# Kernel optimization log

Hardware: AMD Instinct MI355X
Metric: run time of the kernel (lower is better)

## Reference

```python
import jax, jax.numpy as jnp
import numpy as np

B, S, HID = 1, 2048, 4096
NH, NKV = 32, 8
HD = HID // NH            # 128
GROUPS = NH // NKV        # 4
ROPE_THETA = 10000.0


def _rope_cos_sin(seq_len, head_dim, dtype=jnp.float32):
    inv_freq = 1.0 / (ROPE_THETA ** (jnp.arange(0, head_dim, 2, dtype=jnp.float32) / head_dim))
    t = jnp.arange(seq_len, dtype=jnp.float32)
    freqs = jnp.outer(t, inv_freq)                      # [S, HD/2]
    emb = jnp.concatenate([freqs, freqs], axis=-1)      # [S, HD]
    return jnp.cos(emb).astype(dtype), jnp.sin(emb).astype(dtype)


def _rotate_half(x):
    x1, x2 = jnp.split(x, 2, axis=-1)
    return jnp.concatenate([-x2, x1], axis=-1)


def _apply_rope(x, cos, sin):
    # x: [B, H, S, HD]; cos/sin: [S, HD] (position_ids = arange(S), no past)
    return x * cos[None, None] + _rotate_half(x) * sin[None, None]


def setup_inputs() -> dict:
    key = jax.random.key(0)
    k1, k2, k3, k4, k5 = jax.random.split(key, 5)
    return {
        "hidden_states": jax.random.normal(k1, (B, S, HID), jnp.float32),
        "Wq": jax.random.normal(k2, (NH * HD, HID), jnp.float32) * 0.02,
        "Wk": jax.random.normal(k3, (NKV * HD, HID), jnp.float32) * 0.02,
        "Wv": jax.random.normal(k4, (NKV * HD, HID), jnp.float32) * 0.02,
        "Wo": jax.random.normal(k5, (HID, NH * HD), jnp.float32) * 0.02,
    }


def reference(hidden_states, Wq, Wk, Wv, Wo):
    bsz, q_len, _ = hidden_states.shape
    # projections (nn.Linear: x @ W.T)
    q = (hidden_states @ Wq.T).reshape(bsz, q_len, NH, HD).transpose(0, 2, 1, 3)   # [B,NH,S,HD]
    k = (hidden_states @ Wk.T).reshape(bsz, q_len, NKV, HD).transpose(0, 2, 1, 3)  # [B,NKV,S,HD]
    v = (hidden_states @ Wv.T).reshape(bsz, q_len, NKV, HD).transpose(0, 2, 1, 3)

    cos, sin = _rope_cos_sin(q_len, HD, hidden_states.dtype)
    q = _apply_rope(q, cos, sin)
    k = _apply_rope(k, cos, sin)

    # GQA: repeat kv heads (repeat_kv / num_key_value_groups)
    k = jnp.repeat(k, GROUPS, axis=1)   # [B,NH,S,HD]
    v = jnp.repeat(v, GROUPS, axis=1)

    scale = 1.0 / jnp.sqrt(jnp.asarray(HD, hidden_states.dtype))
    logits = jnp.einsum('bhqd,bhkd->bhqk', q, k) * scale   # [B,NH,S,S]

    # prefill causal mask (phys_past_len = 0)
    causal = jnp.tril(jnp.ones((q_len, q_len), dtype=bool))
    logits = jnp.where(causal[None, None], logits, jnp.finfo(logits.dtype).min)

    attn = jax.nn.softmax(logits, axis=-1)
    out = jnp.einsum('bhqk,bhkd->bhqd', attn, v)            # [B,NH,S,HD]
    out = out.transpose(0, 2, 1, 3).reshape(bsz, q_len, NH * HD)
    return out @ Wo.T
```

## Files before the change

kernel.cpp:

```cpp
#include <hip/hip_runtime.h>

typedef __bf16 bf16;
typedef __bf16 bf16x2 __attribute__((ext_vector_type(2)));
typedef __bf16 bf16x4 __attribute__((ext_vector_type(4)));
typedef __bf16 bf16x8 __attribute__((ext_vector_type(8)));
typedef float f32x4 __attribute__((ext_vector_type(4)));

#define S_LEN 2048
#define HID_DIM 4096
#define NH 32
#define NKV 8
#define HD 128
#define QKV_N 6144
#define K_COL 4096
#define V_COL 5120
#define PADV 76

__global__ void cvt_all_kernel(const float* __restrict__ hs, const float* __restrict__ wq,
                               const float* __restrict__ wk, const float* __restrict__ wv,
                               const float* __restrict__ wo, bf16* __restrict__ hsb,
                               bf16* __restrict__ wqkvb, bf16* __restrict__ wob) {
  long i = (long)blockIdx.x * blockDim.x + threadIdx.x;
  const float* src; bf16* dst; long off;
  if (i < 2097152)      { src = hs; dst = hsb;                          off = i; }
  else if (i < 6291456) { src = wq; dst = wqkvb;                        off = i - 2097152; }
  else if (i < 7340032) { src = wk; dst = wqkvb + (long)4096 * 4096;    off = i - 6291456; }
  else if (i < 8388608) { src = wv; dst = wqkvb + (long)5120 * 4096;    off = i - 7340032; }
  else                  { src = wo; dst = wob;                          off = i - 8388608; }
  float4 v = reinterpret_cast<const float4*>(src)[off];
  bf16x4 o;
  o[0] = (bf16)v.x; o[1] = (bf16)v.y; o[2] = (bf16)v.z; o[3] = (bf16)v.w;
  reinterpret_cast<bf16x4*>(dst)[off] = o;
}

__global__ void rope_table_kernel(float* __restrict__ cost, float* __restrict__ sint) {
  int i = blockIdx.x * blockDim.x + threadIdx.x;
  int s = i >> 6, d = i & 63;
  float inv = expf(-0.14391156831212787f * (float)d);
  float ang = (float)s * inv;
  cost[i] = cosf(ang);
  sint[i] = sinf(ang);
}

__global__ void rope_apply_kernel(bf16* __restrict__ qkv, const float* __restrict__ cost,
                                  const float* __restrict__ sint) {
  int idx = blockIdx.x * blockDim.x + threadIdx.x;
  int s = idx / 320;
  int c = idx - s * 320;
  int g = c >> 3, dc = (c & 7) * 8;
  long base = (long)s * QKV_N + g * 128 + dc;
  bf16x8 x1 = *reinterpret_cast<const bf16x8*>(qkv + base);
  bf16x8 x2 = *reinterpret_cast<const bf16x8*>(qkv + base + 64);
  const float* cp = cost + (s << 6) + dc;
  const float* sp = sint + (s << 6) + dc;
  float4 ca = *reinterpret_cast<const float4*>(cp);
  float4 cb = *reinterpret_cast<const float4*>(cp + 4);
  float4 sa = *reinterpret_cast<const float4*>(sp);
  float4 sb = *reinterpret_cast<const float4*>(sp + 4);
  float co[8] = {ca.x, ca.y, ca.z, ca.w, cb.x, cb.y, cb.z, cb.w};
  float sn[8] = {sa.x, sa.y, sa.z, sa.w, sb.x, sb.y, sb.z, sb.w};
  bf16x8 y1, y2;
#pragma unroll
  for (int e = 0; e < 8; ++e) {
    float a = (float)x1[e], b = (float)x2[e];
    y1[e] = (bf16)(a * co[e] - b * sn[e]);
    y2[e] = (bf16)(b * co[e] + a * sn[e]);
  }
  *reinterpret_cast<bf16x8*>(qkv + base)      = y1;
  *reinterpret_cast<bf16x8*>(qkv + base + 64) = y2;
}

#define STG8(buf, mat, kt, unit) {                                                       \
    const bf16* sp_ = (mat) ? Bp : Ap;                                                   \
    int row0_ = ((mat) ? n0 : m0) + (unit) * 64;                                         \
    int lb_ = (buf) * LBUF + (mat) * 16384 + (unit) * 4096;                              \
    int r_ = t >> 3, jl_ = t & 7, jg_ = jl_ ^ (r_ & 7);                                  \
    const bf16* src_ = sp_ + (long)(row0_ + r_) * K + (kt) * 64 + jg_ * 8;               \
    __builtin_amdgcn_global_load_lds((const __attribute__((address_space(1))) void*)src_,\
        (__attribute__((address_space(3))) void*)(L + lb_ + t * 8), 16, 0, 0); }

#define DSA8(buf, mh, ks) {                                                              \
    _Pragma("unroll") for (int mf_ = 0; mf_ < 4; ++mf_) {                                \
      int R_ = wr * 128 + (mh) * 64 + mf_ * 16 + lm;                                     \
      aF[mf_] = *reinterpret_cast<const bf16x8*>(                                        \
          L + (buf) * LBUF + R_ * 64 + ((((ks) * 4 + lg) ^ (R_ & 7)) << 3));             \
    } }

#define DSB8(buf) {                                                                      \
    _Pragma("unroll") for (int ks_ = 0; ks_ < 2; ++ks_)                                  \
      _Pragma("unroll") for (int nf_ = 0; nf_ < NB; ++nf_) {                             \
        int R_ = wc * (NB * 16) + nf_ * 16 + lm;                                         \
        bF[ks_][nf_] = *reinterpret_cast<const bf16x8*>(                                 \
            L + (buf) * LBUF + 16384 + R_ * 64 + (((ks_ * 4 + lg) ^ (R_ & 7)) << 3));    \
      } }

#define MM8(mh, ks) {                                                                    \
    __builtin_amdgcn_s_setprio(1);                                                       \
    _Pragma("unroll") for (int mf_ = 0; mf_ < 4; ++mf_)                                  \
      _Pragma("unroll") for (int nf_ = 0; nf_ < NB; ++nf_)                               \
        acc[(mh) * 4 + mf_][nf_] = __builtin_amdgcn_mfma_f32_16x16x32_bf16(              \
            aF[mf_], bF[ks][nf_], acc[(mh) * 4 + mf_][nf_], 0, 0, 0);                    \
    __builtin_amdgcn_s_setprio(0); }

#define BAR() __builtin_amdgcn_s_barrier()
#define WVM(n) asm volatile("s_waitcnt vmcnt(%0)" :: "i"(n) : "memory")

template<int NB, typename OutT>
__global__ __launch_bounds__(512, 1) void gemm8p_kernel(
    const bf16* __restrict__ Ap, const bf16* __restrict__ Bp, OutT* __restrict__ C,
    int M, int N, int K) {
  constexpr int LBUF = 16384 + NB * 4096;
  __shared__ __align__(16) bf16 L[2 * LBUF];

  int nwg = gridDim.x * gridDim.y;
  int bid = blockIdx.y * gridDim.x + blockIdx.x;
  int cpx = nwg >> 3;
  int swz = (bid & 7) * cpx + (bid >> 3);
  int bxs = swz % gridDim.x, bys = swz / gridDim.x;
  const int n0 = bxs * (NB * 64), m0 = bys * 256;

  const int t = threadIdx.x;
  const int lane = t & 63, w = t >> 6;
  const int wr = w >> 2, wc = w & 3;
  const int lg = lane >> 4, lm = lane & 15;
  const int NT = K >> 6;

  f32x4 acc[8][NB] = {};
  bf16x8 aF[4], bF[2][NB];

  STG8(0, 0, 0, 0); STG8(0, 0, 0, 1); STG8(0, 0, 0, 2); STG8(0, 0, 0, 3);
  STG8(0, 1, 0, 0); if (NB > 1) STG8(0, 1, 0, 1); if (NB > 2) STG8(0, 1, 0, 2);
  STG8(1, 1, 1, 0); if (NB > 1) STG8(1, 1, 1, 1); if (NB > 2) STG8(1, 1, 1, 2);
  WVM(NB);
  BAR();

  for (int I = 0; I < (NT >> 1); ++I) {
    const int tt = 2 * I;
    const bool pf = (I < (NT >> 1) - 1);
    DSA8(0, 0, 0); DSB8(0);
    STG8(1, 0, tt + 1, 0); STG8(1, 0, tt + 1, 1);
    BAR(); MM8(0, 0); BAR();
    DSA8(0, 1, 0);
    STG8(1, 0, tt + 1, 2); STG8(1, 0, tt + 1, 3);
    BAR(); MM8(1, 0); BAR();
    DSA8(0, 0, 1);
    if (pf) { STG8(0, 1, tt + 2, 0); if (NB > 1) STG8(0, 1, tt + 2, 1); }
    BAR(); MM8(0, 1); BAR();
    DSA8(0, 1, 1);
    if (pf) { if (NB > 2) STG8(0, 1, tt + 2, 2); }
    BAR(); MM8(1, 1);
    if (pf) WVM(NB); else WVM(0);
    BAR();
    DSA8(1, 0, 0); DSB8(1);
    if (pf) { STG8(0, 0, tt + 2, 0); STG8(0, 0, tt + 2, 1); }
    BAR(); MM8(0, 0); BAR();
    DSA8(1, 1, 0);
    if (pf) { STG8(0, 0, tt + 2, 2); STG8(0, 0, tt + 2, 3); }
    BAR(); MM8(1, 0); BAR();
    DSA8(1, 0, 1);
    if (pf) { STG8(1, 1, tt + 3, 0); if (NB > 1) STG8(1, 1, tt + 3, 1); }
    BAR(); MM8(0, 1); BAR();
    DSA8(1, 1, 1);
    if (pf) { if (NB > 2) STG8(1, 1, tt + 3, 2); }
    BAR(); MM8(1, 1);
    if (pf) WVM(NB); else WVM(0);
    BAR();
  }

#pragma unroll
  for (int am = 0; am < 8; ++am) {
    int row = m0 + wr * 128 + am * 16 + lg * 4;
#pragma unroll
    for (int nf = 0; nf < NB; ++nf) {
      int col = n0 + wc * (NB * 16) + nf * 16 + lm;
#pragma unroll
      for (int rr = 0; rr < 4; ++rr) {
        if constexpr (sizeof(OutT) == 4) C[(long)(row + rr) * N + col] = acc[am][nf][rr];
        else                             C[(long)(row + rr) * N + col] = (bf16)acc[am][nf][rr];
      }
    }
  }
}

__global__ __launch_bounds__(512, 4) void attn_kernel(const bf16* __restrict__ qkv,
                                                      bf16* __restrict__ out) {
  __shared__ __align__(16) bf16 Ks[2][64 * 128];
  __shared__ __align__(16) bf16 Vt[128 * PADV];

  const int bx = blockIdx.x;
  const int qt = 15 - (bx >> 5);
  const int h = bx & 31;
  const int kvh = h >> 2;
  const int q0 = qt * 128;
  const int t = threadIdx.x, lane = t & 63, w = t >> 6;
  const int lg = lane >> 4, lm = lane & 15;
  const int dchunk = t >> 5, kv2 = t & 31;
  const int kva = kv2 * 2;
  const int k5 = kva & 31;
  const int slot = ((kva >> 5) << 5) | (((k5 >> 2) & 3) << 3) | ((k5 >> 4) << 2) | (k5 & 3);
  const bf16* kbase = qkv + K_COL + kvh * HD;
  const bf16* vbase = qkv + V_COL + kvh * HD;

  const long qrow = q0 + w * 16 + lm;
  bf16x8 qf[4];
#pragma unroll
  for (int ks = 0; ks < 4; ++ks)
    qf[ks] = *reinterpret_cast<const bf16x8*>(qkv + qrow * QKV_N + h * HD + ks * 32 + lg * 8);

  f32x4 o[8];
#pragma unroll
  for (int i = 0; i < 8; ++i) o[i] = f32x4{0.f, 0.f, 0.f, 0.f};
  float mrow = -1e30f, lrow = 0.f;

  bf16x8 a0, a1;
  {
#pragma unroll
    for (int i = 0; i < 2; ++i) {
      int c = i * 512 + t;
      int r = c >> 4, jl = c & 15;
      int jg = jl ^ (r & 15);
      const bf16* src = kbase + (long)r * QKV_N + jg * 8;
      __builtin_amdgcn_global_load_lds((const __attribute__((address_space(1))) void*)src,
                                       (__attribute__((address_space(3))) void*)(Ks[0] + c * 8), 16, 0, 0);
    }
    const bf16* vs = vbase + (long)kva * QKV_N + dchunk * 8;
    a0 = *reinterpret_cast<const bf16x8*>(vs);
    a1 = *reinterpret_cast<const bf16x8*>(vs + QKV_N);
  }

  const int nst = 2 * qt + 2;
  for (int st = 0; st < nst; ++st) {
    const int cur = st & 1;
#pragma unroll
    for (int e = 0; e < 8; ++e) {
      bf16x2 pk; pk[0] = a0[e]; pk[1] = a1[e];
      *reinterpret_cast<bf16x2*>(Vt + (dchunk * 8 + e) * PADV + slot) = pk;
    }
    __syncthreads();

    if (st + 1 < nst) {
      const long kv0n = (long)(st + 1) * 64;
#pragma unroll
      for (int i = 0; i < 2; ++i) {
        int c = i * 512 + t;
        int r = c >> 4, jl = c & 15;
        int jg = jl ^ (r & 15);
        const bf16* src = kbase + (kv0n + r) * QKV_N + jg * 8;
        __builtin_amdgcn_global_load_lds((const __attribute__((address_space(1))) void*)src,
                                         (__attribute__((address_space(3))) void*)(Ks[cur ^ 1] + c * 8), 16, 0, 0);
      }
      const bf16* vs = vbase + (kv0n + kva) * QKV_N + dchunk * 8;
      a0 = *reinterpret_cast<const bf16x8*>(vs);
      a1 = *reinterpret_cast<const bf16x8*>(vs + QKV_N);
    }

    const int kv0 = st * 64;
    const int qg = q0 + w * 16 + lm;
    if (kv0 <= q0 + w * 16 + 15) {
      f32x4 s[4];
#pragma unroll
      for (int cb = 0; cb < 4; ++cb) s[cb] = f32x4{0.f, 0.f, 0.f, 0.f};
      __builtin_amdgcn_s_setprio(1);
#pragma unroll
      for (int ks = 0; ks < 4; ++ks) {
#pragma unroll
        for (int cb = 0; cb < 4; ++cb) {
          bf16x8 kf = *reinterpret_cast<const bf16x8*>(
              Ks[cur] + (cb * 16 + lm) * 128 + (((ks * 4 + lg) ^ lm) << 3));
          s[cb] = __builtin_amdgcn_mfma_f32_16x16x32_bf16(kf, qf[ks], s[cb], 0, 0, 0);
        }
      }
      __builtin_amdgcn_s_setprio(0);

      const float SC = 0.12751742f;
      float sl[4][4];
#pragma unroll
      for (int cb = 0; cb < 4; ++cb)
#pragma unroll
        for (int r = 0; r < 4; ++r) {
          float v = s[cb][r] * SC;
          if (st >= nst - 2 && (kv0 + cb * 16 + lg * 4 + r) > qg) v = -1e30f;
          sl[cb][r] = v;
        }
      float tm = sl[0][0];
#pragma unroll
      for (int cb = 0; cb < 4; ++cb)
#pragma unroll
        for (int r = 0; r < 4; ++r) tm = fmaxf(tm, sl[cb][r]);
      tm = fmaxf(tm, __shfl_xor(tm, 16));
      tm = fmaxf(tm, __shfl_xor(tm, 32));

      if (__any(tm > mrow + 8.f)) {
        float mnew = fmaxf(mrow, tm);
        float alpha = exp2f(mrow - mnew);
        mrow = mnew;
        lrow *= alpha;
        float ar[4];
#pragma unroll
        for (int r = 0; r < 4; ++r)
          ar[r] = __shfl(alpha, (lane & 48) | (lg * 4 + r));
#pragma unroll
        for (int i = 0; i < 8; ++i)
#pragma unroll
          for (int r = 0; r < 4; ++r) o[i][r] *= ar[r];
      }
      float p[4][4];
      float psum = 0.f;
#pragma unroll
      for (int cb = 0; cb < 4; ++cb)
#pragma unroll
        for (int r = 0; r < 4; ++r) {
          p[cb][r] = exp2f(sl[cb][r] - mrow);
          psum += p[cb][r];
        }
      psum += __shfl_xor(psum, 16);
      psum += __shfl_xor(psum, 32);
      lrow += psum;

      bf16x8 pa0, pa1;
#pragma unroll
      for (int r = 0; r < 4; ++r) {
        pa0[r]     = (bf16)p[0][r];
        pa0[4 + r] = (bf16)p[1][r];
        pa1[r]     = (bf16)p[2][r];
        pa1[4 + r] = (bf16)p[3][r];
      }

      __builtin_amdgcn_s_setprio(1);
#pragma unroll
      for (int db = 0; db < 8; ++db) {
        bf16x8 vf0 = *reinterpret_cast<const bf16x8*>(Vt + (db * 16 + lm) * PADV + lg * 8);
        bf16x8 vf1 = *reinterpret_cast<const bf16x8*>(Vt + (db * 16 + lm) * PADV + 32 + lg * 8);
        o[db] = __builtin_amdgcn_mfma_f32_16x16x32_bf16(pa0, vf0, o[db], 0, 0, 0);
        o[db] = __builtin_amdgcn_mfma_f32_16x16x32_bf16(pa1, vf1, o[db], 0, 0, 0);
      }
      __builtin_amdgcn_s_setprio(0);
    }

    if (st + 1 < nst) __syncthreads();
  }

  float invr[4];
#pragma unroll
  for (int r = 0; r < 4; ++r)
    invr[r] = 1.0f / __shfl(lrow, (lane & 48) | (lg * 4 + r));
#pragma unroll
  for (int r = 0; r < 4; ++r) {
    long row = q0 + w * 16 + lg * 4 + r;
#pragma unroll
    for (int db = 0; db < 8; ++db)
      out[row * HID_DIM + h * HD + db * 16 + lm] = (bf16)(o[db][r] * invr[r]);
  }
}

extern "C" void kernel_launch(void* const* d_in, const int* in_sizes, int n_in,
                              void* d_out, int out_size, void* d_ws, size_t ws_size,
                              hipStream_t stream) {
  const float* hs = (const float*)d_in[0];
  const float* Wq = (const float*)d_in[1];
  const float* Wk = (const float*)d_in[2];
  const float* Wv = (const float*)d_in[3];
  const float* Wo = (const float*)d_in[4];
  float* out = (float*)d_out;
  char* ws = (char*)d_ws;

  bf16*  hsb   = (bf16*)(ws);
  bf16*  wqkvb = (bf16*)(ws + 16777216);
  bf16*  wob   = (bf16*)(ws + 67108864);
  bf16*  qkv   = (bf16*)(ws + 100663296);
  bf16*  attn  = (bf16*)(ws + 125829120);
  float* cost  = (float*)(ws + 142606336);
  float* sint  = (float*)(ws + 143130624);

  cvt_all_kernel<<<49152, 256, 0, stream>>>(hs, Wq, Wk, Wv, Wo, hsb, wqkvb, wob);
  rope_table_kernel<<<512, 256, 0, stream>>>(cost, sint);
  gemm8p_kernel<3, bf16><<<dim3(32, 8), 512, 0, stream>>>(hsb, wqkvb, qkv, 2048, 6144, 4096);
  rope_apply_kernel<<<2560, 256, 0, stream>>>(qkv, cost, sint);
  attn_kernel<<<512, 512, 0, stream>>>(qkv, attn);
  gemm8p_kernel<2, float><<<dim3(32, 8), 512, 0, stream>>>(attn, wob, out, 2048, 4096, 4096);
}
```

Before: 310.7 us.

## Cut GEMM pipeline to four phases per K-pair and fuse rope table into convert

The GEMM main loop now loads both k-subslices of A fragments at once and issues MFMAs over both, so each 64-wide K tile needs two barrier-separated phases instead of four. Global-to-LDS prefetches are regrouped to match the new phases. This halves the number of workgroup barriers and LDS-read phases, but raises register pressure because the A fragments double. The rope cos/sin table computation is also folded into the conversion kernel, which removes one kernel launch.

```diff
diff --git a/kernel.cpp b/kernel.cpp
--- a/kernel.cpp
+++ b/kernel.cpp
@@ -19,8 +19,18 @@
 __global__ void cvt_all_kernel(const float* __restrict__ hs, const float* __restrict__ wq,
                                const float* __restrict__ wk, const float* __restrict__ wv,
                                const float* __restrict__ wo, bf16* __restrict__ hsb,
-                               bf16* __restrict__ wqkvb, bf16* __restrict__ wob) {
+                               bf16* __restrict__ wqkvb, bf16* __restrict__ wob,
+                               float* __restrict__ cost, float* __restrict__ sint) {
   long i = (long)blockIdx.x * blockDim.x + threadIdx.x;
+  if (i >= 12582912) {
+    int j = (int)(i - 12582912);
+    int s = j >> 6, d = j & 63;
+    float inv = expf(-0.14391156831212787f * (float)d);
+    float ang = (float)s * inv;
+    cost[j] = cosf(ang);
+    sint[j] = sinf(ang);
+    return;
+  }
   const float* src; bf16* dst; long off;
   if (i < 2097152)      { src = hs; dst = hsb;                          off = i; }
   else if (i < 6291456) { src = wq; dst = wqkvb;                        off = i - 2097152; }
@@ -31,15 +41,6 @@
   bf16x4 o;
   o[0] = (bf16)v.x; o[1] = (bf16)v.y; o[2] = (bf16)v.z; o[3] = (bf16)v.w;
   reinterpret_cast<bf16x4*>(dst)[off] = o;
-}
-
-__global__ void rope_table_kernel(float* __restrict__ cost, float* __restrict__ sint) {
-  int i = blockIdx.x * blockDim.x + threadIdx.x;
-  int s = i >> 6, d = i & 63;
-  float inv = expf(-0.14391156831212787f * (float)d);
-  float ang = (float)s * inv;
-  cost[i] = cosf(ang);
-  sint[i] = sinf(ang);
 }
 
 __global__ void rope_apply_kernel(bf16* __restrict__ qkv, const float* __restrict__ cost,
@@ -79,14 +80,15 @@
     __builtin_amdgcn_global_load_lds((const __attribute__((address_space(1))) void*)src_,\
         (__attribute__((address_space(3))) void*)(L + lb_ + t * 8), 16, 0, 0); }
 
-#define DSA8(buf, mh, ks) {                                                              \
-    _Pragma("unroll") for (int mf_ = 0; mf_ < 4; ++mf_) {                                \
-      int R_ = wr * 128 + (mh) * 64 + mf_ * 16 + lm;                                     \
-      aF[mf_] = *reinterpret_cast<const bf16x8*>(                                        \
-          L + (buf) * LBUF + R_ * 64 + ((((ks) * 4 + lg) ^ (R_ & 7)) << 3));             \
-    } }
-
-#define DSB8(buf) {                                                                      \
+#define DSA2(buf, mh) {                                                                  \
+    _Pragma("unroll") for (int ks_ = 0; ks_ < 2; ++ks_)                                  \
+      _Pragma("unroll") for (int mf_ = 0; mf_ < 4; ++mf_) {                              \
+        int R_ = wr * 128 + (mh) * 64 + mf_ * 16 + lm;                                   \
+        aF[ks_][mf_] = *reinterpret_cast<const bf16x8*>(                                 \
+            L + (buf) * LBUF + R_ * 64 + (((ks_ * 4 + lg) ^ (R_ & 7)) << 3));            \
+      } }
+
+#define DSBALL(buf) {                                                                    \
     _Pragma("unroll") for (int ks_ = 0; ks_ < 2; ++ks_)                                  \
       _Pragma("unroll") for (int nf_ = 0; nf_ < NB; ++nf_) {                             \
         int R_ = wc * (NB * 16) + nf_ * 16 + lm;                                         \
@@ -94,19 +96,20 @@
             L + (buf) * LBUF + 16384 + R_ * 64 + (((ks_ * 4 + lg) ^ (R_ & 7)) << 3));    \
       } }
 
-#define MM8(mh, ks) {                                                                    \
+#define MM2(mh) {                                                                        \
     __builtin_amdgcn_s_setprio(1);                                                       \
     _Pragma("unroll") for (int mf_ = 0; mf_ < 4; ++mf_)                                  \
       _Pragma("unroll") for (int nf_ = 0; nf_ < NB; ++nf_)                               \
-        acc[(mh) * 4 + mf_][nf_] = __builtin_amdgcn_mfma_f32_16x16x32_bf16(              \
-            aF[mf_], bF[ks][nf_], acc[(mh) * 4 + mf_][nf_], 0, 0, 0);                    \
+        _Pragma("unroll") for (int ks_ = 0; ks_ < 2; ++ks_)                              \
+          acc[(mh) * 4 + mf_][nf_] = __builtin_amdgcn_mfma_f32_16x16x32_bf16(            \
+              aF[ks_][mf_], bF[ks_][nf_], acc[(mh) * 4 + mf_][nf_], 0, 0, 0);            \
     __builtin_amdgcn_s_setprio(0); }
 
 #define BAR() __builtin_amdgcn_s_barrier()
 #define WVM(n) asm volatile("s_waitcnt vmcnt(%0)" :: "i"(n) : "memory")
 
 template<int NB, typename OutT>
-__global__ __launch_bounds__(512, 1) void gemm8p_kernel(
+__global__ __launch_bounds__(512, 1) void gemm4p_kernel(
     const bf16* __restrict__ Ap, const bf16* __restrict__ Bp, OutT* __restrict__ C,
     int M, int N, int K) {
   constexpr int LBUF = 16384 + NB * 4096;
@@ -126,7 +129,7 @@
   const int NT = K >> 6;
 
   f32x4 acc[8][NB] = {};
-  bf16x8 aF[4], bF[2][NB];
+  bf16x8 aF[2][4], bF[2][NB];
 
   STG8(0, 0, 0, 0); STG8(0, 0, 0, 1); STG8(0, 0, 0, 2); STG8(0, 0, 0, 3);
   STG8(0, 1, 0, 0); if (NB > 1) STG8(0, 1, 0, 1); if (NB > 2) STG8(0, 1, 0, 2);
@@ -137,32 +140,24 @@
   for (int I = 0; I < (NT >> 1); ++I) {
     const int tt = 2 * I;
     const bool pf = (I < (NT >> 1) - 1);
-    DSA8(0, 0, 0); DSB8(0);
+    DSA2(0, 0); DSBALL(0);
     STG8(1, 0, tt + 1, 0); STG8(1, 0, tt + 1, 1);
-    BAR(); MM8(0, 0); BAR();
-    DSA8(0, 1, 0);
     STG8(1, 0, tt + 1, 2); STG8(1, 0, tt + 1, 3);
-    BAR(); MM8(1, 0); BAR();
-    DSA8(0, 0, 1);
-    if (pf) { STG8(0, 1, tt + 2, 0); if (NB > 1) STG8(0, 1, tt + 2, 1); }
-    BAR(); MM8(0, 1); BAR();
-    DSA8(0, 1, 1);
-    if (pf) { if (NB > 2) STG8(0, 1, tt + 2, 2); }
-    BAR(); MM8(1, 1);
+    BAR(); MM2(0); BAR();
+    DSA2(0, 1);
+    if (pf) { STG8(0, 1, tt + 2, 0); if (NB > 1) STG8(0, 1, tt + 2, 1);
+              if (NB > 2) STG8(0, 1, tt + 2, 2); }
+    BAR(); MM2(1);
     if (pf) WVM(NB); else WVM(0);
     BAR();
-    DSA8(1, 0, 0); DSB8(1);
-    if (pf) { STG8(0, 0, tt + 2, 0); STG8(0, 0, tt + 2, 1); }
-    BAR(); MM8(0, 0); BAR();
-    DSA8(1, 1, 0);
-    if (pf) { STG8(0, 0, tt + 2, 2); STG8(0, 0, tt + 2, 3); }
-    BAR(); MM8(1, 0); BAR();
-    DSA8(1, 0, 1);
-    if (pf) { STG8(1, 1, tt + 3, 0); if (NB > 1) STG8(1, 1, tt + 3, 1); }
-    BAR(); MM8(0, 1); BAR();
-    DSA8(1, 1, 1);
-    if (pf) { if (NB > 2) STG8(1, 1, tt + 3, 2); }
-    BAR(); MM8(1, 1);
+    DSA2(1, 0); DSBALL(1);
+    if (pf) { STG8(0, 0, tt + 2, 0); STG8(0, 0, tt + 2, 1);
+              STG8(0, 0, tt + 2, 2); STG8(0, 0, tt + 2, 3); }
+    BAR(); MM2(0); BAR();
+    DSA2(1, 1);
+    if (pf) { STG8(1, 1, tt + 3, 0); if (NB > 1) STG8(1, 1, tt + 3, 1);
+              if (NB > 2) STG8(1, 1, tt + 3, 2); }
+    BAR(); MM2(1);
     if (pf) WVM(NB); else WVM(0);
     BAR();
   }
@@ -372,10 +367,9 @@
   float* cost  = (float*)(ws + 142606336);
   float* sint  = (float*)(ws + 143130624);
 
-  cvt_all_kernel<<<49152, 256, 0, stream>>>(hs, Wq, Wk, Wv, Wo, hsb, wqkvb, wob);
-  rope_table_kernel<<<512, 256, 0, stream>>>(cost, sint);
-  gemm8p_kernel<3, bf16><<<dim3(32, 8), 512, 0, stream>>>(hsb, wqkvb, qkv, 2048, 6144, 4096);
+  cvt_all_kernel<<<49664, 256, 0, stream>>>(hs, Wq, Wk, Wv, Wo, hsb, wqkvb, wob, cost, sint);
+  gemm4p_kernel<3, bf16><<<dim3(32, 8), 512, 0, stream>>>(hsb, wqkvb, qkv, 2048, 6144, 4096);
   rope_apply_kernel<<<2560, 256, 0, stream>>>(qkv, cost, sint);
   attn_kernel<<<512, 512, 0, stream>>>(qkv, attn);
-  gemm8p_kernel<2, float><<<dim3(32, 8), 512, 0, stream>>>(attn, wob, out, 2048, 4096, 4096);
-}
+  gemm4p_kernel<2, float><<<dim3(32, 8), 512, 0, stream>>>(attn, wob, out, 2048, 4096, 4096);
+}
```

New measurement: 309.2 us. No clear change (-0.5%).
